# Optimization experiments

Measured on AMD Instinct MI355X. Metric: run time of the kernel, lower is better.

## Reference

```python
import jax, jax.numpy as jnp
import numpy as np

D_MODEL = 1024
NUM_HEADS = 16
HEAD_DIM = D_MODEL // NUM_HEADS


def setup_inputs() -> dict:
    key = jax.random.key(0)
    ks = jax.random.split(key, 11)
    B, S = 2, 2048
    sc = 1.0 / np.sqrt(D_MODEL)
    inp = {
        "query": jax.random.normal(ks[0], (B, S, D_MODEL), jnp.float32),
        "key": jax.random.normal(ks[1], (B, S, D_MODEL), jnp.float32),
        "value": jax.random.normal(ks[2], (B, S, D_MODEL), jnp.float32),
        "Wq": jax.random.normal(ks[3], (D_MODEL, D_MODEL), jnp.float32) * sc,
        "bq": jnp.zeros((D_MODEL,), jnp.float32),
        "Wk": jax.random.normal(ks[4], (D_MODEL, D_MODEL), jnp.float32) * sc,
        "bk": jnp.zeros((D_MODEL,), jnp.float32),
        "Wv": jax.random.normal(ks[5], (D_MODEL, D_MODEL), jnp.float32) * sc,
        "bv": jnp.zeros((D_MODEL,), jnp.float32),
        "Wo": jax.random.normal(ks[6], (D_MODEL, D_MODEL), jnp.float32) * sc,
        "bo": jnp.zeros((D_MODEL,), jnp.float32),
    }
    return inp


def _split_heads(x):
    B, S, _ = x.shape
    return x.reshape(B, S, NUM_HEADS, HEAD_DIM).transpose(0, 2, 1, 3)  # [B,H,S,Dh]


def reference(query, key, value, Wq, bq, Wk, bk, Wv, bv, Wo, bo):
    Q = _split_heads(query @ Wq.T + bq)
    K = _split_heads(key @ Wk.T + bk)
    V = _split_heads(value @ Wv.T + bv)
    scores = jnp.einsum("bhqd,bhkd->bhqk", Q, K) / jnp.sqrt(jnp.float32(HEAD_DIM))
    attn = jax.nn.softmax(scores, axis=-1)  # dropout = identity (eval)
    out = jnp.einsum("bhqk,bhkd->bhqd", attn, V)
    B, H, S, Dh = out.shape
    out = out.transpose(0, 2, 1, 3).reshape(B, S, H * Dh)
    return out @ Wo.T + bo
```

## Files before the change

### kernel.cpp

```cpp
#include <hip/hip_runtime.h>
#include <hip/hip_bf16.h>

typedef __attribute__((ext_vector_type(8))) short short8;
typedef __attribute__((ext_vector_type(4))) short short4v;
typedef __attribute__((ext_vector_type(4))) float f32x4;
typedef __attribute__((ext_vector_type(16))) float f32x16;
typedef __attribute__((ext_vector_type(4))) int int4v;
typedef __attribute__((ext_vector_type(2))) int int2v;

#define DEV static __device__ __forceinline__

constexpr int S_LEN   = 2048;
constexpr int DMODEL  = 1024;
constexpr int NHEAD   = 16;
constexpr int DHEAD   = 64;
constexpr int NBATCH  = 2;
constexpr int BHN     = NBATCH * NHEAD;
constexpr int MROWS   = NBATCH * S_LEN;
constexpr int NDIM    = DMODEL;

constexpr float QSCALE = 0.125f * 1.442695041f;

DEV unsigned short f2b(float f) {
  __hip_bfloat16 h = __float2bfloat16(f);
  return __builtin_bit_cast(unsigned short, h);
}
DEV unsigned pk2(float a, float b) {
  return (unsigned)f2b(a) | ((unsigned)f2b(b) << 16);
}
DEV short8 ld8(const void* p) {
  return *reinterpret_cast<const short8*>(p);
}
DEV f32x4 mfma16(short8 a, short8 b, f32x4 c) {
  return __builtin_amdgcn_mfma_f32_16x16x32_bf16(a, b, c, 0, 0, 0);
}
DEV f32x16 mfma32(short8 a, short8 b, f32x16 c) {
  return __builtin_amdgcn_mfma_f32_32x32x16_bf16(a, b, c, 0, 0, 0);
}
DEV void gload16(const void* g, void* l) {
  __builtin_amdgcn_global_load_lds(
      (const __attribute__((address_space(1))) unsigned*)g,
      (__attribute__((address_space(3))) unsigned*)l, 16, 0, 0);
}
DEV float exp2n(float x) {
#if __has_builtin(__builtin_amdgcn_exp2f)
  return __builtin_amdgcn_exp2f(x);
#else
  float r;
  asm("v_exp_f32 %0, %1" : "=v"(r) : "v"(x));
  return r;
#endif
}

struct CvtArgs {
  const float* src[7];
  unsigned short* dst[7];
  int n4[7];
};

__global__ __launch_bounds__(256) void cvt_bf16(CvtArgs c) {
  const int seg = blockIdx.y;
  const float* __restrict__ s = c.src[seg];
  unsigned short* __restrict__ d = c.dst[seg];
  const int n4 = c.n4[seg];
  for (int i = blockIdx.x * 256 + threadIdx.x; i < n4; i += gridDim.x * 256) {
    f32x4 v = reinterpret_cast<const f32x4*>(s)[i];
    short4v r;
    r[0] = (short)f2b(v[0]); r[1] = (short)f2b(v[1]);
    r[2] = (short)f2b(v[2]); r[3] = (short)f2b(v[3]);
    reinterpret_cast<short4v*>(d)[i] = r;
  }
}

struct GB {
  const unsigned short* A[3];
  const unsigned short* W[3];
  const float* bia[3];
  void* out[3];
  int epi[3];
};

__global__ __launch_bounds__(256, 4) void gemm_bf16(GB g) {
  const int cpx = gridDim.x >> 3;
  const int swz = (blockIdx.x & 7) * cpx + (blockIdx.x >> 3);
  const int z   = swz >> 9;
  const int rem = swz & 511;
  const int bm  = rem >> 4, bn = rem & 15;

  const unsigned short* __restrict__ A = g.A[z];
  const unsigned short* __restrict__ W = g.W[z];
  const float* __restrict__ bia = g.bia[z];
  const int epi = g.epi[z];
  const int tid = threadIdx.x, lane = tid & 63, wid = tid >> 6;
  const int wr = wid >> 1, wc = wid & 1;
  const int fr = lane & 15, gq = lane >> 4;

  __shared__ unsigned short As[2][128][32];
  __shared__ unsigned short Bs[2][64][32];

  f32x4 acc[4][2] = {};

  const int srow = lane >> 2;
  const int scol = ((lane & 3) ^ ((srow >> 1) & 3)) * 16;
  const char* aS = (const char*)A + (size_t)(bm * 128 + wid * 32 + srow) * 2048 + scol;
  const char* bS = (const char*)W + (size_t)(bn * 64 + wid * 16 + srow) * 2048 + scol;

  auto stage = [&](int buf, int kt) {
    const int ko = kt * 64;
    char* a0 = (char*)As[buf] + wid * 2048;
    char* b0 = (char*)Bs[buf] + wid * 1024;
    gload16(aS + ko, a0);
    gload16(aS + (size_t)16 * 2048 + ko, a0 + 1024);
    gload16(bS + ko, b0);
  };

  const int rdo = (gq ^ ((fr >> 1) & 3)) * 8;

  stage(0, 0);
  __syncthreads();
  for (int kt = 0; kt < 32; ++kt) {
    const int buf = kt & 1;
    if (kt + 1 < 32) stage(buf ^ 1, kt + 1);
    short8 af[4], bf4[2];
#pragma unroll
    for (int i = 0; i < 4; ++i) af[i] = ld8(&As[buf][wr * 64 + i * 16 + fr][rdo]);
#pragma unroll
    for (int j = 0; j < 2; ++j) bf4[j] = ld8(&Bs[buf][wc * 32 + j * 16 + fr][rdo]);
#pragma unroll
    for (int i = 0; i < 4; ++i)
#pragma unroll
      for (int j = 0; j < 2; ++j)
        acc[i][j] = mfma16(af[i], bf4[j], acc[i][j]);
    __syncthreads();
  }

#pragma unroll
  for (int i = 0; i < 4; ++i) {
#pragma unroll
    for (int j = 0; j < 2; ++j) {
#pragma unroll
      for (int r = 0; r < 4; ++r) {
        const int row = bm * 128 + wr * 64 + i * 16 + gq * 4 + r;
        const int col = bn * 64 + wc * 32 + j * 16 + fr;
        float v = acc[i][j][r] + bia[col];
        if (epi == 3) {
          ((float*)g.out[z])[(size_t)row * NDIM + col] = v;
        } else {
          const int b = row >> 11, s = row & (S_LEN - 1);
          const int h = col >> 6,  dh = col & (DHEAD - 1);
          unsigned short* O = (unsigned short*)g.out[z];
          if (epi == 0)      O[((size_t)(b * NHEAD + h) * S_LEN + s) * DHEAD + dh] = f2b(v * QSCALE);
          else if (epi == 1) O[((size_t)(b * NHEAD + h) * S_LEN + s) * DHEAD + dh] = f2b(v);
          else               O[((size_t)(b * NHEAD + h) * DHEAD + dh) * S_LEN + s] = f2b(v);
        }
      }
    }
  }
}

__global__ __launch_bounds__(512, 2) void attn_fwd(
    const unsigned short* __restrict__ Qp,
    const unsigned short* __restrict__ Kp,
    const unsigned short* __restrict__ Vt,
    unsigned short* __restrict__ AO) {
  const int nb = (blockIdx.x & 7) * 64 + (blockIdx.x >> 3);
  const int qt = nb & 15, bh = nb >> 4;
  const int tid = threadIdx.x, lane = tid & 63, wid = tid >> 6;
  const int qw = wid & 3, hw = wid >> 2;
  const int ql = lane & 31, hi = lane >> 5, l7 = lane & 7, l3 = lane >> 3;

  const unsigned short* Qh = Qp + (size_t)bh * S_LEN * DHEAD;
  const char* Kh = (const char*)(Kp + (size_t)bh * S_LEN * DHEAD);
  const char* Vh = (const char*)(Vt + (size_t)bh * DHEAD * S_LEN);

  __shared__ unsigned short Klds[2][2][4096];
  __shared__ unsigned short Vlds[2][2][4096];

  const int q0 = qt * 128 + qw * 32;
  short8 qf[4];
#pragma unroll
  for (int d16 = 0; d16 < 4; ++d16)
    qf[d16] = ld8(Qh + (size_t)(q0 + ql) * DHEAD + d16 * 16 + hi * 8);

  const int swc = (l7 ^ l3) << 4;
  const char* kS = Kh + (size_t)hw * 16 * 8192 + (qw * 16 + l3) * 128 + swc;
  const char* vS = Vh + (size_t)hw * 16 * 128 + (qw * 16 + l3) * 4096 + swc;
  char* kD0 = (char*)Klds[hw][0] + qw * 2048;
  char* vD0 = (char*)Vlds[hw][0] + qw * 2048;
  char* kD1 = (char*)Klds[hw][1] + qw * 2048;
  char* vD1 = (char*)Vlds[hw][1] + qw * 2048;

  int xo[4];
#pragma unroll
  for (int j = 0; j < 4; ++j) xo[j] = ((j * 2 + hi) ^ l7) << 4;

  float lacc[8] = {};
  f32x16 o0 = {}, o1 = {};

  gload16(kS, kD0); gload16(kS + 1024, kD0 + 1024);
  gload16(vS, vD0); gload16(vS + 32768, vD0 + 1024);
  __syncthreads();

  constexpr int NT = S_LEN / 64 / 2;
  for (int kt = 0; kt < NT; ++kt) {
    const int buf = kt & 1;
    if (kt + 1 < NT) {
      const char* kn = kS + (kt + 1) * 8192;
      const char* vn = vS + (kt + 1) * 128;
      char* kD = buf ? kD0 : kD1;
      char* vD = buf ? vD0 : vD1;
      gload16(kn, kD); gload16(kn + 1024, kD + 1024);
      gload16(vn, vD); gload16(vn + 32768, vD + 1024);
    }
    const char* kb = (const char*)Klds[hw][buf] + ql * 128;
    const char* vb = (const char*)Vlds[hw][buf] + ql * 128;

    f32x16 st0 = {}, st1 = {};
#pragma unroll
    for (int d16 = 0; d16 < 4; ++d16) {
      short8 k0 = ld8(kb + xo[d16]);
      short8 k1 = ld8(kb + 4096 + xo[d16]);
      st0 = mfma32(k0, qf[d16], st0);
      st1 = mfma32(k1, qf[d16], st1);
    }

#pragma unroll
    for (int r = 0; r < 16; ++r) {
      st0[r] = exp2n(st0[r]);
      st1[r] = exp2n(st1[r]);
    }
#pragma unroll
    for (int r = 0; r < 8; ++r)
      lacc[r] += (st0[r] + st0[r + 8]) + (st1[r] + st1[r + 8]);

#pragma unroll
    for (int ks = 0; ks < 4; ++ks) {
      const f32x16& p = (ks < 2) ? st0 : st1;
      const int a = 8 * (ks & 1);
      unsigned w0 = pk2(p[a + 0], p[a + 1]);
      unsigned w1 = pk2(p[a + 2], p[a + 3]);
      unsigned w2 = pk2(p[a + 4], p[a + 5]);
      unsigned w3 = pk2(p[a + 6], p[a + 7]);
      unsigned x0 = (unsigned)__shfl_xor((int)w0, 32);
      unsigned x1 = (unsigned)__shfl_xor((int)w1, 32);
      unsigned x2 = (unsigned)__shfl_xor((int)w2, 32);
      unsigned x3 = (unsigned)__shfl_xor((int)w3, 32);
      int4v pi;
      pi[0] = (int)(hi ? x2 : w0);
      pi[1] = (int)(hi ? x3 : w1);
      pi[2] = (int)(hi ? w2 : x0);
      pi[3] = (int)(hi ? w3 : x1);
      short8 pb = __builtin_bit_cast(short8, pi);
      short8 v0 = ld8(vb + xo[ks]);
      short8 v1 = ld8(vb + 4096 + xo[ks]);
      o0 = mfma32(v0, pb, o0);
      o1 = mfma32(v1, pb, o1);
    }
    __syncthreads();
  }

#pragma unroll
  for (int s = 4; s; s >>= 1)
#pragma unroll
    for (int r = 0; r < s; ++r) lacc[r] += lacc[r + s];
  float l = lacc[0] + __shfl_xor(lacc[0], 32);

  float* Kf = (float*)&Klds[0][0][0];
  float* Vf = (float*)&Vlds[0][0][0];
  if (hw == 1) {
#pragma unroll
    for (int r = 0; r < 16; ++r) {
      Kf[qw * 2048 + r * 64 + lane]        = o0[r];
      Kf[qw * 2048 + (16 + r) * 64 + lane] = o1[r];
    }
    Vf[qw * 64 + lane] = l;
  }
  __syncthreads();
  if (hw == 0) {
    const float inv = 1.f / (l + Vf[qw * 64 + lane]);
    const int b = bh >> 4, h = bh & 15;
    unsigned short* Op = AO + ((size_t)(b * S_LEN + q0 + ql)) * DMODEL + h * DHEAD;
#pragma unroll
    for (int gidx = 0; gidx < 4; ++gidx) {
      float f0[4], f1[4];
#pragma unroll
      for (int r = 0; r < 4; ++r) {
        const int rr = gidx * 4 + r;
        f0[r] = (o0[rr] + Kf[qw * 2048 + rr * 64 + lane]) * inv;
        f1[r] = (o1[rr] + Kf[qw * 2048 + (16 + rr) * 64 + lane]) * inv;
      }
      int2v s0, s1;
      s0[0] = (int)pk2(f0[0], f0[1]); s0[1] = (int)pk2(f0[2], f0[3]);
      s1[0] = (int)pk2(f1[0], f1[1]); s1[1] = (int)pk2(f1[2], f1[3]);
      *reinterpret_cast<int2v*>(Op + 8 * gidx + 4 * hi)      = s0;
      *reinterpret_cast<int2v*>(Op + 32 + 8 * gidx + 4 * hi) = s1;
    }
  }
}

extern "C" void kernel_launch(void* const* d_in, const int* in_sizes, int n_in,
                              void* d_out, int out_size, void* d_ws, size_t ws_size,
                              hipStream_t stream) {
  const float* query = (const float*)d_in[0];
  const float* key   = (const float*)d_in[1];
  const float* value = (const float*)d_in[2];
  const float* Wq = (const float*)d_in[3];  const float* bq = (const float*)d_in[4];
  const float* Wk = (const float*)d_in[5];  const float* bk = (const float*)d_in[6];
  const float* Wv = (const float*)d_in[7];  const float* bv = (const float*)d_in[8];
  const float* Wo = (const float*)d_in[9];  const float* bo = (const float*)d_in[10];

  const size_t MB = 1024u * 1024u;
  unsigned short* Xb  = (unsigned short*)((char*)d_ws + 0 * MB);
  unsigned short* Wb  = (unsigned short*)((char*)d_ws + 24 * MB);
  unsigned short* Wob = (unsigned short*)((char*)d_ws + 30 * MB);
  unsigned short* Qp  = (unsigned short*)((char*)d_ws + 32 * MB);
  unsigned short* Kp  = (unsigned short*)((char*)d_ws + 40 * MB);
  unsigned short* Vt  = (unsigned short*)((char*)d_ws + 48 * MB);
  unsigned short* AOb = (unsigned short*)((char*)d_ws + 0 * MB);

  const int NACT = MROWS * DMODEL;
  const int NWT  = DMODEL * DMODEL;

  CvtArgs ca;
  ca.src[0] = query; ca.dst[0] = Xb;            ca.n4[0] = NACT / 4;
  ca.src[1] = key;   ca.dst[1] = Xb + NACT;     ca.n4[1] = NACT / 4;
  ca.src[2] = value; ca.dst[2] = Xb + 2 * NACT; ca.n4[2] = NACT / 4;
  ca.src[3] = Wq;    ca.dst[3] = Wb;            ca.n4[3] = NWT / 4;
  ca.src[4] = Wk;    ca.dst[4] = Wb + NWT;      ca.n4[4] = NWT / 4;
  ca.src[5] = Wv;    ca.dst[5] = Wb + 2 * NWT;  ca.n4[5] = NWT / 4;
  ca.src[6] = Wo;    ca.dst[6] = Wob;           ca.n4[6] = NWT / 4;
  cvt_bf16<<<dim3(512, 7), 256, 0, stream>>>(ca);

  GB g1;
  g1.A[0] = Xb;            g1.A[1] = Xb + NACT; g1.A[2] = Xb + 2 * NACT;
  g1.W[0] = Wb;            g1.W[1] = Wb + NWT;  g1.W[2] = Wb + 2 * NWT;
  g1.bia[0] = bq;  g1.bia[1] = bk; g1.bia[2] = bv;
  g1.out[0] = Qp;  g1.out[1] = Kp; g1.out[2] = Vt;
  g1.epi[0] = 0;   g1.epi[1] = 1;  g1.epi[2] = 2;
  gemm_bf16<<<dim3(16 * 32 * 3), 256, 0, stream>>>(g1);

  attn_fwd<<<dim3(BHN * 16), 512, 0, stream>>>(Qp, Kp, Vt, AOb);

  GB g2 = {};
  g2.A[0] = AOb; g2.W[0] = Wob; g2.bia[0] = bo; g2.out[0] = d_out; g2.epi[0] = 3;
  gemm_bf16<<<dim3(16 * 32), 256, 0, stream>>>(g2);
}
```

Measured before the change: 152.3 us.

## Stage GEMM tiles through registers instead of direct global-to-LDS loads

Replaces the direct global-to-LDS 16-byte loads in the projection GEMM with a register-staged pipeline. Tiles are loaded into registers two iterations ahead and written into the swizzled LDS double buffer one iteration ahead. The swizzle moves from the global source address to the LDS write address, so global reads become contiguous. This costs extra VGPRs and explicit LDS stores, and may lose the async behaviour of direct loads.

Result: no change. 152.0 us (-0.2%).

```diff
diff --git a/kernel.cpp b/kernel.cpp
--- a/kernel.cpp
+++ b/kernel.cpp
@@ -101,26 +101,37 @@
   f32x4 acc[4][2] = {};
 
   const int srow = lane >> 2;
-  const int scol = ((lane & 3) ^ ((srow >> 1) & 3)) * 16;
-  const char* aS = (const char*)A + (size_t)(bm * 128 + wid * 32 + srow) * 2048 + scol;
-  const char* bS = (const char*)W + (size_t)(bn * 64 + wid * 16 + srow) * 2048 + scol;
-
-  auto stage = [&](int buf, int kt) {
+  const int c4   = lane & 3;
+  const char* aS = (const char*)A + (size_t)(bm * 128 + wid * 32 + srow) * 2048 + c4 * 16;
+  const char* bS = (const char*)W + (size_t)(bn * 64 + wid * 16 + srow) * 2048 + c4 * 16;
+  const int swc = (c4 ^ ((srow >> 1) & 3)) * 16;
+  char* aW0 = (char*)&As[0][wid * 32 + srow][0] + swc;
+  char* aW1 = (char*)&As[0][wid * 32 + 16 + srow][0] + swc;
+  char* bW  = (char*)&Bs[0][wid * 16 + srow][0] + swc;
+
+  int4v ra0, ra1, rb;
+  auto LOAD = [&](int kt) {
     const int ko = kt * 64;
-    char* a0 = (char*)As[buf] + wid * 2048;
-    char* b0 = (char*)Bs[buf] + wid * 1024;
-    gload16(aS + ko, a0);
-    gload16(aS + (size_t)16 * 2048 + ko, a0 + 1024);
-    gload16(bS + ko, b0);
+    ra0 = *reinterpret_cast<const int4v*>(aS + ko);
+    ra1 = *reinterpret_cast<const int4v*>(aS + (size_t)16 * 2048 + ko);
+    rb  = *reinterpret_cast<const int4v*>(bS + ko);
   };
+  auto WRITE = [&](int buf) {
+    *reinterpret_cast<int4v*>(aW0 + buf * 8192) = ra0;
+    *reinterpret_cast<int4v*>(aW1 + buf * 8192) = ra1;
+    *reinterpret_cast<int4v*>(bW  + buf * 4096) = rb;
+  };
 
   const int rdo = (gq ^ ((fr >> 1) & 3)) * 8;
 
-  stage(0, 0);
+  LOAD(0);
+  WRITE(0);
+  LOAD(1);
   __syncthreads();
   for (int kt = 0; kt < 32; ++kt) {
     const int buf = kt & 1;
-    if (kt + 1 < 32) stage(buf ^ 1, kt + 1);
+    if (kt + 1 < 32) WRITE(buf ^ 1);
+    if (kt + 2 < 32) LOAD(kt + 2);
     short8 af[4], bf4[2];
 #pragma unroll
     for (int i = 0; i < 4; ++i) af[i] = ld8(&As[buf][wr * 64 + i * 16 + fr][rdo]);
```

## Use single-wave GEMM blocks with 4-stage LDS pipeline and explicit waitcnt

Applied to the files above, without the earlier changes.

The projection GEMM kernel goes from 256-thread blocks with 128x64 tiles and double buffering to 64-thread single-wave blocks with 64x64 tiles and a 4-deep ring of async global-to-LDS loads. Because each block is one wave, __syncthreads is removed and synchronization uses explicit vmcnt/lgkmcnt waits with inline ds_read_b128. The goal is to hide global-load latency with deeper prefetch and to drop barrier overhead. In exchange each wave keeps more accumulator state, the grid is four times larger, and per-block reuse of loaded data is lower.

Measured after the change: 170.1 us. 11.7% more time.

```diff
diff --git a/kernel.cpp b/kernel.cpp
--- a/kernel.cpp
+++ b/kernel.cpp
@@ -51,6 +51,15 @@
   return r;
 #endif
 }
+DEV short8 dsread16(unsigned addr) {
+  short8 d;
+  asm volatile("ds_read_b128 %0, %1" : "=v"(d) : "v"(addr));
+  return d;
+}
+#define WAITV(n)  asm volatile("s_waitcnt vmcnt(" #n ")" ::: "memory")
+#define WAITLGK0  do { asm volatile("s_waitcnt lgkmcnt(0)" ::: "memory"); \
+                       __builtin_amdgcn_sched_barrier(0); } while (0)
+DEV unsigned ldsaddr(const void* p) { return (unsigned)(uintptr_t)p; }
 
 struct CvtArgs {
   const float* src[7];
@@ -80,68 +89,80 @@
   int epi[3];
 };
 
-__global__ __launch_bounds__(256, 4) void gemm_bf16(GB g) {
+__global__ __launch_bounds__(64) void gemm_bf16(GB g) {
   const int cpx = gridDim.x >> 3;
   const int swz = (blockIdx.x & 7) * cpx + (blockIdx.x >> 3);
-  const int z   = swz >> 9;
-  const int rem = swz & 511;
+  const int z   = swz >> 10;
+  const int rem = swz & 1023;
   const int bm  = rem >> 4, bn = rem & 15;
 
   const unsigned short* __restrict__ A = g.A[z];
   const unsigned short* __restrict__ W = g.W[z];
   const float* __restrict__ bia = g.bia[z];
   const int epi = g.epi[z];
-  const int tid = threadIdx.x, lane = tid & 63, wid = tid >> 6;
-  const int wr = wid >> 1, wc = wid & 1;
+  const int lane = threadIdx.x & 63;
   const int fr = lane & 15, gq = lane >> 4;
 
-  __shared__ unsigned short As[2][128][32];
-  __shared__ unsigned short Bs[2][64][32];
-
-  f32x4 acc[4][2] = {};
+  __shared__ unsigned short As[4][64][32];
+  __shared__ unsigned short Bs[4][64][32];
+
+  f32x4 acc[4][4] = {};
 
   const int srow = lane >> 2;
-  const int scol = ((lane & 3) ^ ((srow >> 1) & 3)) * 16;
-  const char* aS = (const char*)A + (size_t)(bm * 128 + wid * 32 + srow) * 2048 + scol;
-  const char* bS = (const char*)W + (size_t)(bn * 64 + wid * 16 + srow) * 2048 + scol;
+  const int c4   = lane & 3;
+  const int csrc = (c4 ^ ((srow >> 1) & 3)) * 16;
+  const char* aS = (const char*)A + (size_t)(bm * 64 + srow) * 2048 + csrc;
+  const char* bS = (const char*)W + (size_t)(bn * 64 + srow) * 2048 + csrc;
 
   auto stage = [&](int buf, int kt) {
     const int ko = kt * 64;
-    char* a0 = (char*)As[buf] + wid * 2048;
-    char* b0 = (char*)Bs[buf] + wid * 1024;
-    gload16(aS + ko, a0);
-    gload16(aS + (size_t)16 * 2048 + ko, a0 + 1024);
-    gload16(bS + ko, b0);
+    char* a0 = (char*)As[buf];
+    char* b0 = (char*)Bs[buf];
+#pragma unroll
+    for (int r = 0; r < 4; ++r) {
+      gload16(aS + (size_t)(r * 16) * 2048 + ko, a0 + r * 1024);
+      gload16(bS + (size_t)(r * 16) * 2048 + ko, b0 + r * 1024);
+    }
   };
 
   const int rdo = (gq ^ ((fr >> 1) & 3)) * 8;
+  unsigned aAd[4], bAd[4];
+#pragma unroll
+  for (int i = 0; i < 4; ++i) {
+    aAd[i] = ldsaddr(&As[0][i * 16 + fr][rdo]);
+    bAd[i] = ldsaddr(&Bs[0][i * 16 + fr][rdo]);
+  }
 
   stage(0, 0);
-  __syncthreads();
+  stage(1, 1);
+  stage(2, 2);
   for (int kt = 0; kt < 32; ++kt) {
-    const int buf = kt & 1;
-    if (kt + 1 < 32) stage(buf ^ 1, kt + 1);
-    short8 af[4], bf4[2];
-#pragma unroll
-    for (int i = 0; i < 4; ++i) af[i] = ld8(&As[buf][wr * 64 + i * 16 + fr][rdo]);
-#pragma unroll
-    for (int j = 0; j < 2; ++j) bf4[j] = ld8(&Bs[buf][wc * 32 + j * 16 + fr][rdo]);
+    if (kt < 30)      { WAITV(16); }
+    else if (kt == 30){ WAITV(8);  }
+    else              { WAITV(0);  }
+    if (kt + 3 < 32) stage((kt + 3) & 3, kt + 3);
+    const unsigned bo = (unsigned)(kt & 3) * 4096;
+    short8 af[4], bf4[4];
+#pragma unroll
+    for (int i = 0; i < 4; ++i) af[i] = dsread16(aAd[i] + bo);
+#pragma unroll
+    for (int j = 0; j < 4; ++j) bf4[j] = dsread16(bAd[j] + bo);
+    WAITLGK0;
 #pragma unroll
     for (int i = 0; i < 4; ++i)
 #pragma unroll
-      for (int j = 0; j < 2; ++j)
+      for (int j = 0; j < 4; ++j)
         acc[i][j] = mfma16(af[i], bf4[j], acc[i][j]);
-    __syncthreads();
   }
 
 #pragma unroll
   for (int i = 0; i < 4; ++i) {
 #pragma unroll
-    for (int j = 0; j < 2; ++j) {
+    for (int j = 0; j < 4; ++j) {
 #pragma unroll
       for (int r = 0; r < 4; ++r) {
-        const int row = bm * 128 + wr * 64 + i * 16 + gq * 4 + r;
-        const int col = bn * 64 + wc * 32 + j * 16 + fr;
+        const int row = bm * 64 + i * 16 + gq * 4 + r;
+        const int col = bn * 64 + j * 16 + fr;
         float v = acc[i][j][r] + bia[col];
         if (epi == 3) {
           ((float*)g.out[z])[(size_t)row * NDIM + col] = v;
@@ -337,11 +358,11 @@
   g1.bia[0] = bq;  g1.bia[1] = bk; g1.bia[2] = bv;
   g1.out[0] = Qp;  g1.out[1] = Kp; g1.out[2] = Vt;
   g1.epi[0] = 0;   g1.epi[1] = 1;  g1.epi[2] = 2;
-  gemm_bf16<<<dim3(16 * 32 * 3), 256, 0, stream>>>(g1);
+  gemm_bf16<<<dim3(64 * 16 * 3), 64, 0, stream>>>(g1);
 
   attn_fwd<<<dim3(BHN * 16), 512, 0, stream>>>(Qp, Kp, Vt, AOb);
 
   GB g2 = {};
   g2.A[0] = AOb; g2.W[0] = Wob; g2.bia[0] = bo; g2.out[0] = d_out; g2.epi[0] = 3;
-  gemm_bf16<<<dim3(16 * 32), 256, 0, stream>>>(g2);
-}
+  gemm_bf16<<<dim3(64 * 16), 64, 0, stream>>>(g2);
+}
```
